# Performance work log

Hardware: AMD Instinct MI355X
Metric: run time of the kernel (lower is better)

## Reference

```python
import jax, jax.numpy as jnp
import numpy as np

H = 512   # hidden_dim
D = 512   # token feature dim (GRU input_size)
A = 256   # attn_dim
V = 10000 # vocab_size
TE = 256  # encoder timesteps
TD = 128  # decoder timesteps


def setup_inputs() -> dict:
    key = jax.random.key(0)
    ks = jax.random.split(key, 18)
    f = lambda k, shape, s: jax.random.normal(k, shape, jnp.float32) * s
    return {
        "x": f(ks[0], (1, TE, D), 1.0),
        "y": f(ks[1], (1, TD, D), 1.0),
        # encoder GRU params (PyTorch layout: gates [r|z|n] stacked)
        "Wi_e": f(ks[2], (3 * H, D), 0.04), "Wh_e": f(ks[3], (3 * H, H), 0.04),
        "bi_e": f(ks[4], (3 * H,), 0.04), "bh_e": f(ks[5], (3 * H,), 0.04),
        # decoder GRU params
        "Wi_d": f(ks[6], (3 * H, D), 0.04), "Wh_d": f(ks[7], (3 * H, H), 0.04),
        "bi_d": f(ks[8], (3 * H,), 0.04), "bh_d": f(ks[9], (3 * H,), 0.04),
        # additive attention params
        "Wh_attn": f(ks[10], (A, H), 0.06), "Ws_attn": f(ks[11], (A, H), 0.06),
        "b_attn": f(ks[12], (A,), 0.06), "v_attn": f(ks[13], (A,), 0.06),
        # output projections
        "W1": f(ks[14], (2 * V, 2 * H), 0.03), "b1": f(ks[15], (2 * V,), 0.03),
        "W2": f(ks[16], (V, 2 * V), 0.02), "b2": f(ks[17], (V,), 0.02),
    }


def _gru_gates(gi, gh, h):
    # gi/gh: [..., 3H] stacked input/hidden gate pre-activations, h: [..., H]
    ir, iz, inn = jnp.split(gi, 3, axis=-1)
    hr, hz, hn = jnp.split(gh, 3, axis=-1)
    r = jax.nn.sigmoid(ir + hr)
    z = jax.nn.sigmoid(iz + hz)
    n = jnp.tanh(inn + r * hn)
    return (1.0 - z) * n + z * h


def reference(x, y, Wi_e, Wh_e, bi_e, bh_e, Wi_d, Wh_d, bi_d, bh_d,
              Wh_attn, Ws_attn, b_attn, v_attn, W1, b1, W2, b2):
    X = x[0]  # [TE, D]
    Y = y[0]  # [TD, D]

    # Encoder: original calls self.encoder per single token with NO carried
    # hidden state, so each h_i is one GRU step from zero hidden. Vectorized:
    gi = X @ Wi_e.T + bi_e                      # [TE, 3H]
    gh = jnp.broadcast_to(bh_e, gi.shape)       # zero hidden -> only bias
    enc_H = _gru_gates(gi, gh, jnp.zeros((X.shape[0], H), X.dtype))  # [TE, H]
    h0 = enc_H[-1]                              # encoder_hidden_last

    # Decoder GRU over y with initial hidden h0
    def step(h, x_t):
        gi_t = x_t @ Wi_d.T + bi_d
        gh_t = h @ Wh_d.T + bh_d
        h_new = _gru_gates(gi_t, gh_t, h)
        return h_new, h_new

    _, dec_S = jax.lax.scan(step, h0, Y)        # [TD, H]

    # Bahdanau additive attention, fully batched over (TD, TE)
    encP = enc_H @ Wh_attn.T                    # [TE, A]
    decP = dec_S @ Ws_attn.T                    # [TD, A]
    e = jnp.tanh(encP[None, :, :] + decP[:, None, :] + b_attn)  # [TD, TE, A]
    scores = jnp.einsum('tea,a->te', e, v_attn)  # [TD, TE]
    attn = jax.nn.softmax(scores, axis=1)        # softmax over encoder steps
    context = attn @ enc_H                       # [TD, H]

    concat = jnp.concatenate([context, dec_S], axis=-1)  # [TD, 2H]
    out = concat @ W1.T + b1                     # [TD, 2V]
    out = out @ W2.T + b2                        # [TD, V]
    return out
```

## Files before the change

### kernel.cpp

```cpp
#include <hip/hip_runtime.h>
#include <stdint.h>

#define HID 512
#define THREE_H 1536
#define ADIM 256
#define NVOC 10000
#define TEnc 256
#define TDec 128

typedef float f32x4 __attribute__((ext_vector_type(4)));
typedef __bf16 bf16x8 __attribute__((ext_vector_type(8)));

__device__ __forceinline__ unsigned short f2bf(float f) {
  union { float f; unsigned u; } v; v.f = f;
  unsigned r = v.u + 0x7FFFu + ((v.u >> 16) & 1u);
  return (unsigned short)(r >> 16);
}
__device__ __forceinline__ float sigmoidf_(float x) { return 1.f / (1.f + __expf(-x)); }
__device__ __forceinline__ float tanh_fast(float x) {
  float ax = fabsf(x);
  float e = __expf(ax + ax);
  float t = 1.f - 2.f / (e + 1.f);
  return copysignf(t, x);
}

#define GLDS16(gp, lp)                                                                 \
  __builtin_amdgcn_global_load_lds((const __attribute__((address_space(1))) void*)(gp),\
                                   (__attribute__((address_space(3))) void*)(lp), 16, 0, 0)

__global__ void cvt_f32_bf16(const float* __restrict__ in, unsigned short* __restrict__ out, int n) {
  int i = (blockIdx.x * blockDim.x + threadIdx.x) * 4;
  if (i < n) {
    float4 v = *(const float4*)(in + i);
    ushort4 o;
    o.x = f2bf(v.x); o.y = f2bf(v.y); o.z = f2bf(v.z); o.w = f2bf(v.w);
    *(ushort4*)(out + i) = o;
  }
}

template <int BN, int BK>
__global__ __launch_bounds__(256, 1) void gemm_bt(
    const unsigned short* __restrict__ Abf, const float* __restrict__ B,
    const float* __restrict__ bias, float* __restrict__ C, unsigned short* __restrict__ Cbf,
    int M, int N, int K) {
  constexpr int NF = BN / 16;
  constexpr int B4 = BN * BK / 1024;
  constexpr int AG = BK / 16;
  constexpr int KK = BK / 32;
  extern __shared__ char smem[];
  unsigned short* Al0 = (unsigned short*)smem;
  unsigned short* Al1 = Al0 + 128 * BK;
  unsigned short* Bl0 = Al1 + 128 * BK;
  unsigned short* Bl1 = Bl0 + BN * BK;

  const int tid = threadIdx.x;
  const int lane = tid & 63;
  const int wid = tid >> 6;
  const int m0 = blockIdx.x * 128;
  const int n0 = blockIdx.y * BN;
  const int NT = K / BK;

  float4 breg[B4];
  f32x4 acc[2][NF];
#pragma unroll
  for (int i = 0; i < 2; ++i)
#pragma unroll
    for (int j = 0; j < NF; ++j) acc[i][j] = (f32x4){0.f, 0.f, 0.f, 0.f};

  auto stageA = [&](int t, unsigned short* dst) {
    const unsigned short* Ab = Abf + (size_t)m0 * K + (size_t)t * BK;
#pragma unroll
    for (int g = 0; g < AG; ++g) {
      int elem = g * 2048 + tid * 8;
      int arow = elem / BK;
      int acol = elem - arow * BK;
      GLDS16(Ab + (size_t)arow * K + acol, (char*)dst + g * 4096 + wid * 1024);
    }
  };
  auto loadB = [&](int t) {
    const float* Bb = B + (size_t)t * BK;
#pragma unroll
    for (int p = 0; p < B4; ++p) {
      int e = (p * 256 + tid) * 4;
      int brow = e / BK;
      int bcol = e - brow * BK;
      int grow = n0 + brow;
      if (grow > N - 1) grow = N - 1;
      breg[p] = *(const float4*)(Bb + (size_t)grow * K + bcol);
    }
  };
  auto writeB = [&](unsigned short* dst) {
#pragma unroll
    for (int p = 0; p < B4; ++p) {
      ushort4 o;
      o.x = f2bf(breg[p].x); o.y = f2bf(breg[p].y);
      o.z = f2bf(breg[p].z); o.w = f2bf(breg[p].w);
      *(ushort4*)((char*)dst + (p * 256 + tid) * 8) = o;
    }
  };

  stageA(0, Al0);
  loadB(0);
  for (int t = 0; t < NT; ++t) {
    unsigned short* Ac = (t & 1) ? Al1 : Al0;
    unsigned short* Bc = (t & 1) ? Bl1 : Bl0;
    asm volatile("s_waitcnt vmcnt(0)" ::: "memory");
    writeB(Bc);
    __syncthreads();
    if (t + 1 < NT) {
      stageA(t + 1, (t & 1) ? Al0 : Al1);
      loadB(t + 1);
    }
    const int r0 = lane & 15;
    const int kb = (lane >> 4) * 8;
#pragma unroll
    for (int kk = 0; kk < KK; ++kk) {
      int ko = kk * 32 + kb;
      bf16x8 a0 = *(const bf16x8*)(Ac + (wid * 32 + r0) * BK + ko);
      bf16x8 a1 = *(const bf16x8*)(Ac + (wid * 32 + 16 + r0) * BK + ko);
#pragma unroll
      for (int nf = 0; nf < NF; ++nf) {
        bf16x8 bb = *(const bf16x8*)(Bc + (nf * 16 + r0) * BK + ko);
        acc[0][nf] = __builtin_amdgcn_mfma_f32_16x16x32_bf16(a0, bb, acc[0][nf], 0, 0, 0);
        acc[1][nf] = __builtin_amdgcn_mfma_f32_16x16x32_bf16(a1, bb, acc[1][nf], 0, 0, 0);
      }
    }
  }
  const int cc = lane & 15;
  const int rq = (lane >> 4) * 4;
#pragma unroll
  for (int mi = 0; mi < 2; ++mi) {
    int row = m0 + wid * 32 + mi * 16 + rq;
#pragma unroll
    for (int nf = 0; nf < NF; ++nf) {
      int col = n0 + nf * 16 + cc;
      if (col < N) {
        float bv = bias ? bias[col] : 0.f;
#pragma unroll
        for (int j = 0; j < 4; ++j) {
          float v = acc[mi][nf][j] + bv;
          if (C) C[(size_t)(row + j) * N + col] = v;
          if (Cbf) Cbf[(size_t)(row + j) * N + col] = f2bf(v);
        }
      }
    }
  }
}

__global__ __launch_bounds__(256) void enc_gate(const float* __restrict__ giX,
                                                const float* __restrict__ bie,
                                                const float* __restrict__ bhe,
                                                float* __restrict__ encH,
                                                unsigned short* __restrict__ encHbf) {
  int idx = blockIdx.x * 256 + threadIdx.x;
  int i = idx >> 9, j = idx & 511;
  const float* gi = giX + (size_t)i * THREE_H;
  float r = sigmoidf_(gi[j] + bie[j] + bhe[j]);
  float z = sigmoidf_(gi[HID + j] + bie[HID + j] + bhe[HID + j]);
  float n = tanh_fast(gi[2 * HID + j] + bie[2 * HID + j] + r * bhe[2 * HID + j]);
  float h = (1.f - z) * n;
  encH[idx] = h;
  encHbf[idx] = f2bf(h);
}

__global__ __launch_bounds__(256, 1) void gru_scan_xcd(
    const float* __restrict__ Whd, const float* __restrict__ bhd,
    const float* __restrict__ giY, const float* __restrict__ h0,
    unsigned long long* __restrict__ hx, unsigned int* __restrict__ cnt,
    unsigned int* __restrict__ winner,
    unsigned short* __restrict__ decSbf, unsigned short* __restrict__ concatbf) {
  extern __shared__ char smem[];
  float* WT = (float*)smem;
  float* hl = WT + 48 * 512;
  float* dots = hl + 512;
  const int tid = threadIdx.x;
  const int lane = tid & 63, wid = tid >> 6;
  volatile int* slot_sh = (volatile int*)(dots + 52);

  if (tid == 0) {
    unsigned xcd;
    asm volatile("s_getreg_b32 %0, hwreg(20, 0, 32)" : "=s"(xcd));
    xcd &= 7u;
    unsigned slot = atomicAdd(&cnt[xcd], 1u);
    if (slot == 31u) atomicCAS(winner, 0u, xcd + 1u);
    unsigned win = 0;
    if (slot < 32u) {
      int spin = 0;
      while ((win = __hip_atomic_load(winner, __ATOMIC_RELAXED,
                                      __HIP_MEMORY_SCOPE_AGENT)) == 0u &&
             ++spin < (1 << 20))
        __builtin_amdgcn_s_sleep(2);
    }
    *slot_sh = (slot < 32u && win == xcd + 1u) ? (int)slot : -1;
  }
  __syncthreads();
  const int g = *slot_sh;
  if (g < 0) return;

  for (int idx = tid * 4; idx < 48 * 512; idx += 1024) {
    int rr = idx >> 9;
    int ccl = idx & 511;
    int grow = (rr >> 4) * HID + g * 16 + (rr & 15);
    float4 w4 = *(const float4*)(Whd + (size_t)grow * HID + ccl);
    *(float4*)(WT + ((ccl >> 2) * 48 + rr) * 4) = w4;
  }
  if (tid < 128) *(float4*)(hl + tid * 4) = *(const float4*)(h0 + tid * 4);
  __syncthreads();

  volatile unsigned long long* hxv = (volatile unsigned long long*)hx;

  for (int t = 0; t < TDec; ++t) {
    if (wid < 3) {
      int row = wid * 16 + (lane & 15);
      int q = lane >> 4;
      const float4* wp = (const float4*)WT;
      const float4* hp = (const float4*)hl;
      float p = 0.f;
#pragma unroll 8
      for (int k4 = q * 32; k4 < q * 32 + 32; ++k4) {
        float4 wv = wp[k4 * 48 + row];
        float4 hv = hp[k4];
        p += wv.x * hv.x + wv.y * hv.y + wv.z * hv.z + wv.w * hv.w;
      }
      p += __shfl_xor(p, 16);
      p += __shfl_xor(p, 32);
      if (lane < 16) dots[row] = p;
    }
    __syncthreads();
    if (tid < 16) {
      int j = g * 16 + tid;
      const float* gi = giY + (size_t)t * THREE_H;
      float r = sigmoidf_(gi[j] + dots[tid] + bhd[j]);
      float z = sigmoidf_(gi[HID + j] + dots[16 + tid] + bhd[HID + j]);
      float n = tanh_fast(gi[2 * HID + j] + r * (dots[32 + tid] + bhd[2 * HID + j]));
      float hn = (1.f - z) * n + z * hl[j];
      hxv[j] = ((unsigned long long)(unsigned)(t + 1) << 32) |
               (unsigned long long)__float_as_uint(hn);
      unsigned short hb = f2bf(hn);
      decSbf[(size_t)t * HID + j] = hb;
      concatbf[(size_t)t * 2 * HID + HID + j] = hb;
    }
    if (t == TDec - 1) break;
    __syncthreads();
    unsigned long long w0, w1;
    int spin = 0;
    do { w0 = hxv[tid]; } while ((unsigned)(w0 >> 32) != (unsigned)(t + 1) && ++spin < (1 << 16));
    spin = 0;
    do { w1 = hxv[tid + 256]; } while ((unsigned)(w1 >> 32) != (unsigned)(t + 1) && ++spin < (1 << 16));
    hl[tid] = __uint_as_float((unsigned)w0);
    hl[tid + 256] = __uint_as_float((unsigned)w1);
    __syncthreads();
  }
}

__global__ __launch_bounds__(256) void attn_ctx(const float* __restrict__ encP,
                                                const float* __restrict__ decP,
                                                const float* __restrict__ vattn,
                                                const float* __restrict__ encH,
                                                unsigned short* __restrict__ concatbf) {
  __shared__ float dp[ADIM], vv[ADIM], pl[TEnc];
  __shared__ float red[8];
  const int t = blockIdx.x, tid = threadIdx.x;
  if (tid < 64) {
    *(float4*)(dp + tid * 4) = *(const float4*)(decP + (size_t)t * ADIM + tid * 4);
    *(float4*)(vv + tid * 4) = *(const float4*)(vattn + tid * 4);
  }
  __syncthreads();
  float s = 0.f;
  const float* ep = encP + (size_t)tid * ADIM;
#pragma unroll 4
  for (int a = 0; a < ADIM; a += 4) {
    float4 e4 = *(const float4*)(ep + a);
    s += vv[a] * tanh_fast(e4.x + dp[a]);
    s += vv[a + 1] * tanh_fast(e4.y + dp[a + 1]);
    s += vv[a + 2] * tanh_fast(e4.z + dp[a + 2]);
    s += vv[a + 3] * tanh_fast(e4.w + dp[a + 3]);
  }
  float m = s;
#pragma unroll
  for (int off = 32; off; off >>= 1) m = fmaxf(m, __shfl_xor(m, off));
  if ((tid & 63) == 0) red[tid >> 6] = m;
  __syncthreads();
  m = fmaxf(fmaxf(red[0], red[1]), fmaxf(red[2], red[3]));
  float p = __expf(s - m);
  pl[tid] = p;
  float sum = p;
#pragma unroll
  for (int off = 32; off; off >>= 1) sum += __shfl_xor(sum, off);
  if ((tid & 63) == 0) red[4 + (tid >> 6)] = sum;
  __syncthreads();
  float inv = 1.f / (red[4] + red[5] + red[6] + red[7]);
  float a0 = 0.f, a1 = 0.f;
  for (int e = 0; e < TEnc; ++e) {
    float pe = pl[e];
    a0 += pe * encH[(size_t)e * HID + tid];
    a1 += pe * encH[(size_t)e * HID + tid + 256];
  }
  concatbf[(size_t)t * 2 * HID + tid] = f2bf(a0 * inv);
  concatbf[(size_t)t * 2 * HID + tid + 256] = f2bf(a1 * inv);
}

extern "C" void kernel_launch(void* const* d_in, const int* in_sizes, int n_in,
                              void* d_out, int out_size, void* d_ws, size_t ws_size,
                              hipStream_t stream) {
  const float* x = (const float*)d_in[0];
  const float* y = (const float*)d_in[1];
  const float* Wi_e = (const float*)d_in[2];
  const float* bi_e = (const float*)d_in[4];
  const float* bh_e = (const float*)d_in[5];
  const float* Wi_d = (const float*)d_in[6];
  const float* Wh_d = (const float*)d_in[7];
  const float* bi_d = (const float*)d_in[8];
  const float* bh_d = (const float*)d_in[9];
  const float* Wh_attn = (const float*)d_in[10];
  const float* Ws_attn = (const float*)d_in[11];
  const float* b_attn = (const float*)d_in[12];
  const float* v_attn = (const float*)d_in[13];
  const float* W1 = (const float*)d_in[14];
  const float* b1 = (const float*)d_in[15];
  const float* W2 = (const float*)d_in[16];
  const float* b2 = (const float*)d_in[17];
  float* out = (float*)d_out;

  char* ws = (char*)d_ws;
  size_t off = 0;
  auto alloc = [&](size_t bytes) {
    char* p = ws + off;
    off += (bytes + 255) & ~(size_t)255;
    return p;
  };
  char* ctrl = alloc(8192);
  unsigned long long* hx = (unsigned long long*)ctrl;
  unsigned int* cnt = (unsigned int*)(ctrl + 4096);
  unsigned int* winner = (unsigned int*)(ctrl + 4096 + 128);
  unsigned short* Xbf = (unsigned short*)alloc((size_t)TEnc * HID * 2);
  unsigned short* Ybf = (unsigned short*)alloc((size_t)TDec * HID * 2);
  float* giX = (float*)alloc((size_t)TEnc * THREE_H * 4);
  float* giY = (float*)alloc((size_t)TDec * THREE_H * 4);
  float* encH = (float*)alloc((size_t)TEnc * HID * 4);
  unsigned short* encHbf = (unsigned short*)alloc((size_t)TEnc * HID * 2);
  float* encP = (float*)alloc((size_t)TEnc * ADIM * 4);
  float* decP = (float*)alloc((size_t)TDec * ADIM * 4);
  unsigned short* decSbf = (unsigned short*)alloc((size_t)TDec * HID * 2);
  unsigned short* concatbf = (unsigned short*)alloc((size_t)TDec * 2 * HID * 2);
  unsigned short* out1bf = (unsigned short*)alloc((size_t)TDec * 20000 * 2);

  hipMemsetAsync(ctrl, 0, 8192, stream);

  auto* g32 = gemm_bt<32, 128>;
  auto* g80 = gemm_bt<80, 128>;
  auto* g64 = gemm_bt<64, 160>;
  const int smem32 = (128 + 32) * 128 * 2 * 2;
  const int smem80 = (128 + 80) * 128 * 2 * 2;
  const int smem64 = (128 + 64) * 160 * 2 * 2;
  const int smemScan = (48 * 512 + 512 + 64) * 4;
  hipFuncSetAttribute((const void*)g32, hipFuncAttributeMaxDynamicSharedMemorySize, smem32);
  hipFuncSetAttribute((const void*)g80, hipFuncAttributeMaxDynamicSharedMemorySize, smem80);
  hipFuncSetAttribute((const void*)g64, hipFuncAttributeMaxDynamicSharedMemorySize, smem64);
  hipFuncSetAttribute((const void*)gru_scan_xcd, hipFuncAttributeMaxDynamicSharedMemorySize, smemScan);

  cvt_f32_bf16<<<TEnc * HID / 1024, 256, 0, stream>>>(x, Xbf, TEnc * HID);
  cvt_f32_bf16<<<TDec * HID / 1024, 256, 0, stream>>>(y, Ybf, TDec * HID);

  g32<<<dim3(2, 48), 256, smem32, stream>>>(Xbf, Wi_e, nullptr, giX, nullptr, 256, 1536, 512);
  enc_gate<<<TEnc * HID / 256, 256, 0, stream>>>(giX, bi_e, bh_e, encH, encHbf);
  g32<<<dim3(2, 8), 256, smem32, stream>>>(encHbf, Wh_attn, nullptr, encP, nullptr, 256, 256, 512);
  g32<<<dim3(1, 48), 256, smem32, stream>>>(Ybf, Wi_d, bi_d, giY, nullptr, 128, 1536, 512);
  gru_scan_xcd<<<256, 256, smemScan, stream>>>(Wh_d, bh_d, giY, encH + 255 * HID,
                                               hx, cnt, winner, decSbf, concatbf);
  g32<<<dim3(1, 8), 256, smem32, stream>>>(decSbf, Ws_attn, b_attn, decP, nullptr, 128, 256, 512);
  attn_ctx<<<TDec, 256, 0, stream>>>(encP, decP, v_attn, encH, concatbf);
  g80<<<dim3(1, 250), 256, smem80, stream>>>(concatbf, W1, b1, nullptr, out1bf, 128, 20000, 1024);
  g64<<<dim3(1, 157), 256, smem64, stream>>>(out1bf, W2, b2, out, nullptr, 128, 10000, 20000);
}
```

Baseline: 664.7 us.

## Fuse encoder gates into GEMM epilogue, register-resident GRU weights, merge conversions

The encoder input GEMM now computes r/z/n columns for the same hidden units in one tile and applies the GRU gate math in its epilogue, which removes the giX intermediate and the separate enc_gate launch. The two f32→bf16 conversion launches are merged into one. The decoder scan keeps each block's Wh slice in registers instead of LDS, pads h in LDS, and hands the gate math and polling of the cross-block hidden-state exchange to a dedicated fourth wave, trimming per-step barriers. The cost is more register pressure from 32 float4 weights per lane, and the scan still requests a large dynamic LDS allocation that now goes mostly unused.

After: 753.9 us. 13.4% more time.

```diff
diff --git a/kernel.cpp b/kernel.cpp
--- a/kernel.cpp
+++ b/kernel.cpp
@@ -28,14 +28,18 @@
   __builtin_amdgcn_global_load_lds((const __attribute__((address_space(1))) void*)(gp),\
                                    (__attribute__((address_space(3))) void*)(lp), 16, 0, 0)
 
-__global__ void cvt_f32_bf16(const float* __restrict__ in, unsigned short* __restrict__ out, int n) {
+__global__ void cvt_xy(const float* __restrict__ x, const float* __restrict__ y,
+                       unsigned short* __restrict__ xb, unsigned short* __restrict__ yb) {
   int i = (blockIdx.x * blockDim.x + threadIdx.x) * 4;
-  if (i < n) {
-    float4 v = *(const float4*)(in + i);
-    ushort4 o;
-    o.x = f2bf(v.x); o.y = f2bf(v.y); o.z = f2bf(v.z); o.w = f2bf(v.w);
-    *(ushort4*)(out + i) = o;
-  }
+  const float* src;
+  unsigned short* dst;
+  int j;
+  if (i < TEnc * HID) { src = x; dst = xb; j = i; }
+  else { src = y; dst = yb; j = i - TEnc * HID; }
+  float4 v = *(const float4*)(src + j);
+  ushort4 o;
+  o.x = f2bf(v.x); o.y = f2bf(v.y); o.z = f2bf(v.z); o.w = f2bf(v.w);
+  *(ushort4*)(dst + j) = o;
 }
 
 template <int BN, int BK>
@@ -147,20 +151,112 @@
   }
 }
 
-__global__ __launch_bounds__(256) void enc_gate(const float* __restrict__ giX,
-                                                const float* __restrict__ bie,
-                                                const float* __restrict__ bhe,
-                                                float* __restrict__ encH,
-                                                unsigned short* __restrict__ encHbf) {
-  int idx = blockIdx.x * 256 + threadIdx.x;
-  int i = idx >> 9, j = idx & 511;
-  const float* gi = giX + (size_t)i * THREE_H;
-  float r = sigmoidf_(gi[j] + bie[j] + bhe[j]);
-  float z = sigmoidf_(gi[HID + j] + bie[HID + j] + bhe[HID + j]);
-  float n = tanh_fast(gi[2 * HID + j] + bie[2 * HID + j] + r * bhe[2 * HID + j]);
-  float h = (1.f - z) * n;
-  encH[idx] = h;
-  encHbf[idx] = f2bf(h);
+__global__ __launch_bounds__(256, 1) void gemm_enc(
+    const unsigned short* __restrict__ Abf, const float* __restrict__ Wi,
+    const float* __restrict__ bi, const float* __restrict__ bh,
+    float* __restrict__ encH, unsigned short* __restrict__ encHbf) {
+  constexpr int BN = 96, BK = 128, NF = 6, B4 = 12, AG = 8, KK = 4, K = 512;
+  extern __shared__ char smem[];
+  unsigned short* Al0 = (unsigned short*)smem;
+  unsigned short* Al1 = Al0 + 128 * BK;
+  unsigned short* Bl0 = Al1 + 128 * BK;
+  unsigned short* Bl1 = Bl0 + BN * BK;
+
+  const int tid = threadIdx.x;
+  const int lane = tid & 63;
+  const int wid = tid >> 6;
+  const int m0 = blockIdx.x * 128;
+  const int n0g = blockIdx.y * 32;
+  const int NT = K / BK;
+
+  float4 breg[B4];
+  f32x4 acc[2][NF];
+#pragma unroll
+  for (int i = 0; i < 2; ++i)
+#pragma unroll
+    for (int j = 0; j < NF; ++j) acc[i][j] = (f32x4){0.f, 0.f, 0.f, 0.f};
+
+  auto stageA = [&](int t, unsigned short* dst) {
+    const unsigned short* Ab = Abf + (size_t)m0 * K + (size_t)t * BK;
+#pragma unroll
+    for (int g = 0; g < AG; ++g) {
+      int elem = g * 2048 + tid * 8;
+      int arow = elem >> 7;
+      int acol = elem & 127;
+      GLDS16(Ab + (size_t)arow * K + acol, (char*)dst + g * 4096 + wid * 1024);
+    }
+  };
+  auto loadB = [&](int t) {
+    const float* Bb = Wi + (size_t)t * BK;
+#pragma unroll
+    for (int p = 0; p < B4; ++p) {
+      int e = (p * 256 + tid) * 4;
+      int brow = e >> 7;
+      int bcol = e & 127;
+      int grow = (brow >> 5) * HID + n0g + (brow & 31);
+      breg[p] = *(const float4*)(Bb + (size_t)grow * K + bcol);
+    }
+  };
+  auto writeB = [&](unsigned short* dst) {
+#pragma unroll
+    for (int p = 0; p < B4; ++p) {
+      ushort4 o;
+      o.x = f2bf(breg[p].x); o.y = f2bf(breg[p].y);
+      o.z = f2bf(breg[p].z); o.w = f2bf(breg[p].w);
+      *(ushort4*)((char*)dst + (p * 256 + tid) * 8) = o;
+    }
+  };
+
+  stageA(0, Al0);
+  loadB(0);
+  for (int t = 0; t < NT; ++t) {
+    unsigned short* Ac = (t & 1) ? Al1 : Al0;
+    unsigned short* Bc = (t & 1) ? Bl1 : Bl0;
+    asm volatile("s_waitcnt vmcnt(0)" ::: "memory");
+    writeB(Bc);
+    __syncthreads();
+    if (t + 1 < NT) {
+      stageA(t + 1, (t & 1) ? Al0 : Al1);
+      loadB(t + 1);
+    }
+    const int r0 = lane & 15;
+    const int kb = (lane >> 4) * 8;
+#pragma unroll
+    for (int kk = 0; kk < KK; ++kk) {
+      int ko = kk * 32 + kb;
+      bf16x8 a0 = *(const bf16x8*)(Ac + (wid * 32 + r0) * BK + ko);
+      bf16x8 a1 = *(const bf16x8*)(Ac + (wid * 32 + 16 + r0) * BK + ko);
+#pragma unroll
+      for (int nf = 0; nf < NF; ++nf) {
+        bf16x8 bb = *(const bf16x8*)(Bc + (nf * 16 + r0) * BK + ko);
+        acc[0][nf] = __builtin_amdgcn_mfma_f32_16x16x32_bf16(a0, bb, acc[0][nf], 0, 0, 0);
+        acc[1][nf] = __builtin_amdgcn_mfma_f32_16x16x32_bf16(a1, bb, acc[1][nf], 0, 0, 0);
+      }
+    }
+  }
+  const int cc = lane & 15;
+  const int rq = (lane >> 4) * 4;
+#pragma unroll
+  for (int mi = 0; mi < 2; ++mi) {
+    int row = m0 + wid * 32 + mi * 16 + rq;
+#pragma unroll
+    for (int nfj = 0; nfj < 2; ++nfj) {
+      int j = n0g + nfj * 16 + cc;
+      float br_ = bi[j] + bh[j];
+      float bz_ = bi[HID + j] + bh[HID + j];
+      float bin_ = bi[2 * HID + j];
+      float bhn_ = bh[2 * HID + j];
+#pragma unroll
+      for (int jj = 0; jj < 4; ++jj) {
+        float r = sigmoidf_(acc[mi][nfj][jj] + br_);
+        float z = sigmoidf_(acc[mi][nfj + 2][jj] + bz_);
+        float n = tanh_fast(acc[mi][nfj + 4][jj] + bin_ + r * bhn_);
+        float h = (1.f - z) * n;
+        encH[(size_t)(row + jj) * HID + j] = h;
+        encHbf[(size_t)(row + jj) * HID + j] = f2bf(h);
+      }
+    }
+  }
 }
 
 __global__ __launch_bounds__(256, 1) void gru_scan_xcd(
@@ -170,12 +266,11 @@
     unsigned int* __restrict__ winner,
     unsigned short* __restrict__ decSbf, unsigned short* __restrict__ concatbf) {
   extern __shared__ char smem[];
-  float* WT = (float*)smem;
-  float* hl = WT + 48 * 512;
-  float* dots = hl + 512;
+  float* hl = (float*)smem;
+  float* dots = hl + 544;
+  volatile int* slot_sh = (volatile int*)(dots + 48);
   const int tid = threadIdx.x;
   const int lane = tid & 63, wid = tid >> 6;
-  volatile int* slot_sh = (volatile int*)(dots + 52);
 
   if (tid == 0) {
     unsigned xcd;
@@ -197,59 +292,95 @@
   const int g = *slot_sh;
   if (g < 0) return;
 
-  for (int idx = tid * 4; idx < 48 * 512; idx += 1024) {
-    int rr = idx >> 9;
-    int ccl = idx & 511;
-    int grow = (rr >> 4) * HID + g * 16 + (rr & 15);
-    float4 w4 = *(const float4*)(Whd + (size_t)grow * HID + ccl);
-    *(float4*)(WT + ((ccl >> 2) * 48 + rr) * 4) = w4;
-  }
-  if (tid < 128) *(float4*)(hl + tid * 4) = *(const float4*)(h0 + tid * 4);
-  __syncthreads();
+  const int row16 = lane & 15;
+  const int q = lane >> 4;
+
+  float4 wreg[32];
+  if (wid < 3) {
+    const float* wr = Whd + ((size_t)wid * HID + (size_t)g * 16 + row16) * HID + q * 128;
+#pragma unroll
+    for (int i = 0; i < 32; ++i) wreg[i] = *(const float4*)(wr + i * 4);
+  }
+  float bhr = 0.f, bhz = 0.f, bhn = 0.f;
+  if (wid == 3 && lane < 16) {
+    int j = g * 16 + lane;
+    bhr = bhd[j]; bhz = bhd[HID + j]; bhn = bhd[2 * HID + j];
+  }
+  if (wid == 3) {
+#pragma unroll
+    for (int k = 0; k < 8; ++k) {
+      int w = lane + (k << 6);
+      hl[w + ((w >> 7) << 2)] = h0[w];
+    }
+  }
 
   volatile unsigned long long* hxv = (volatile unsigned long long*)hx;
+  float gir = 0.f, giz = 0.f, gin = 0.f;
 
   for (int t = 0; t < TDec; ++t) {
+    __syncthreads();
     if (wid < 3) {
-      int row = wid * 16 + (lane & 15);
-      int q = lane >> 4;
-      const float4* wp = (const float4*)WT;
       const float4* hp = (const float4*)hl;
-      float p = 0.f;
-#pragma unroll 8
-      for (int k4 = q * 32; k4 < q * 32 + 32; ++k4) {
-        float4 wv = wp[k4 * 48 + row];
-        float4 hv = hp[k4];
-        p += wv.x * hv.x + wv.y * hv.y + wv.z * hv.z + wv.w * hv.w;
-      }
+      const int hb = q * 33;
+      float p0 = 0.f, p1 = 0.f, p2 = 0.f, p3 = 0.f;
+#pragma unroll
+      for (int i = 0; i < 32; i += 4) {
+        float4 ha = hp[hb + i], hv = hp[hb + i + 1], hc = hp[hb + i + 2], hd = hp[hb + i + 3];
+        float4 wa = wreg[i], wb = wreg[i + 1], wc = wreg[i + 2], wd = wreg[i + 3];
+        p0 += wa.x * ha.x + wa.y * ha.y + wa.z * ha.z + wa.w * ha.w;
+        p1 += wb.x * hv.x + wb.y * hv.y + wb.z * hv.z + wb.w * hv.w;
+        p2 += wc.x * hc.x + wc.y * hc.y + wc.z * hc.z + wc.w * hc.w;
+        p3 += wd.x * hd.x + wd.y * hd.y + wd.z * hd.z + wd.w * hd.w;
+      }
+      float p = (p0 + p1) + (p2 + p3);
       p += __shfl_xor(p, 16);
       p += __shfl_xor(p, 32);
-      if (lane < 16) dots[row] = p;
+      if (lane < 16) dots[wid * 16 + lane] = p;
+    } else if (lane < 16) {
+      int j = g * 16 + lane;
+      const float* gi = giY + (size_t)t * THREE_H;
+      gir = gi[j]; giz = gi[HID + j]; gin = gi[2 * HID + j];
     }
     __syncthreads();
-    if (tid < 16) {
-      int j = g * 16 + tid;
-      const float* gi = giY + (size_t)t * THREE_H;
-      float r = sigmoidf_(gi[j] + dots[tid] + bhd[j]);
-      float z = sigmoidf_(gi[HID + j] + dots[16 + tid] + bhd[HID + j]);
-      float n = tanh_fast(gi[2 * HID + j] + r * (dots[32 + tid] + bhd[2 * HID + j]));
-      float hn = (1.f - z) * n + z * hl[j];
-      hxv[j] = ((unsigned long long)(unsigned)(t + 1) << 32) |
-               (unsigned long long)__float_as_uint(hn);
-      unsigned short hb = f2bf(hn);
-      decSbf[(size_t)t * HID + j] = hb;
-      concatbf[(size_t)t * 2 * HID + HID + j] = hb;
-    }
-    if (t == TDec - 1) break;
-    __syncthreads();
-    unsigned long long w0, w1;
-    int spin = 0;
-    do { w0 = hxv[tid]; } while ((unsigned)(w0 >> 32) != (unsigned)(t + 1) && ++spin < (1 << 16));
-    spin = 0;
-    do { w1 = hxv[tid + 256]; } while ((unsigned)(w1 >> 32) != (unsigned)(t + 1) && ++spin < (1 << 16));
-    hl[tid] = __uint_as_float((unsigned)w0);
-    hl[tid + 256] = __uint_as_float((unsigned)w1);
-    __syncthreads();
+    if (wid == 3) {
+      if (lane < 16) {
+        int j = g * 16 + lane;
+        float hprev = hl[j + ((j >> 7) << 2)];
+        float r = sigmoidf_(gir + dots[lane] + bhr);
+        float z = sigmoidf_(giz + dots[16 + lane] + bhz);
+        float n = tanh_fast(gin + r * (dots[32 + lane] + bhn));
+        float hn = (1.f - z) * n + z * hprev;
+        hxv[j] = ((unsigned long long)(unsigned)(t + 1) << 32) |
+                 (unsigned long long)__float_as_uint(hn);
+        unsigned short hb16 = f2bf(hn);
+        decSbf[(size_t)t * HID + j] = hb16;
+        concatbf[(size_t)t * 2 * HID + HID + j] = hb16;
+      }
+      if (t < TDec - 1) {
+        unsigned need = 0xFFu;
+        unsigned long long got[8];
+        got[0]=0;got[1]=0;got[2]=0;got[3]=0;got[4]=0;got[5]=0;got[6]=0;got[7]=0;
+        int guard = 0;
+        while (need && ++guard < (1 << 20)) {
+#pragma unroll
+          for (int k = 0; k < 8; ++k) {
+            if (need & (1u << k)) {
+              unsigned long long w = hxv[lane + (k << 6)];
+              if ((unsigned)(w >> 32) == (unsigned)(t + 1)) {
+                got[k] = w;
+                need &= ~(1u << k);
+              }
+            }
+          }
+          if (need) __builtin_amdgcn_s_sleep(1);
+        }
+#pragma unroll
+        for (int k = 0; k < 8; ++k) {
+          int w = lane + (k << 6);
+          hl[w + ((w >> 7) << 2)] = __uint_as_float((unsigned)got[k]);
+        }
+      }
+    }
   }
 }
 
@@ -335,7 +466,6 @@
   unsigned int* winner = (unsigned int*)(ctrl + 4096 + 128);
   unsigned short* Xbf = (unsigned short*)alloc((size_t)TEnc * HID * 2);
   unsigned short* Ybf = (unsigned short*)alloc((size_t)TDec * HID * 2);
-  float* giX = (float*)alloc((size_t)TEnc * THREE_H * 4);
   float* giY = (float*)alloc((size_t)TDec * THREE_H * 4);
   float* encH = (float*)alloc((size_t)TEnc * HID * 4);
   unsigned short* encHbf = (unsigned short*)alloc((size_t)TEnc * HID * 2);
@@ -353,17 +483,16 @@
   const int smem32 = (128 + 32) * 128 * 2 * 2;
   const int smem80 = (128 + 80) * 128 * 2 * 2;
   const int smem64 = (128 + 64) * 160 * 2 * 2;
-  const int smemScan = (48 * 512 + 512 + 64) * 4;
+  const int smemEnc = (128 + 96) * 128 * 2 * 2;
+  const int smemScan = 100608;
   hipFuncSetAttribute((const void*)g32, hipFuncAttributeMaxDynamicSharedMemorySize, smem32);
   hipFuncSetAttribute((const void*)g80, hipFuncAttributeMaxDynamicSharedMemorySize, smem80);
   hipFuncSetAttribute((const void*)g64, hipFuncAttributeMaxDynamicSharedMemorySize, smem64);
+  hipFuncSetAttribute((const void*)gemm_enc, hipFuncAttributeMaxDynamicSharedMemorySize, smemEnc);
   hipFuncSetAttribute((const void*)gru_scan_xcd, hipFuncAttributeMaxDynamicSharedMemorySize, smemScan);
 
-  cvt_f32_bf16<<<TEnc * HID / 1024, 256, 0, stream>>>(x, Xbf, TEnc * HID);
-  cvt_f32_bf16<<<TDec * HID / 1024, 256, 0, stream>>>(y, Ybf, TDec * HID);
-
-  g32<<<dim3(2, 48), 256, smem32, stream>>>(Xbf, Wi_e, nullptr, giX, nullptr, 256, 1536, 512);
-  enc_gate<<<TEnc * HID / 256, 256, 0, stream>>>(giX, bi_e, bh_e, encH, encHbf);
+  cvt_xy<<<(TEnc + TDec) * HID / 1024, 256, 0, stream>>>(x, y, Xbf, Ybf);
+  gemm_enc<<<dim3(2, 16), 256, smemEnc, stream>>>(Xbf, Wi_e, bi_e, bh_e, encH, encHbf);
   g32<<<dim3(2, 8), 256, smem32, stream>>>(encHbf, Wh_attn, nullptr, encP, nullptr, 256, 256, 512);
   g32<<<dim3(1, 48), 256, smem32, stream>>>(Ybf, Wi_d, bi_d, giY, nullptr, 128, 1536, 512);
   gru_scan_xcd<<<256, 256, smemScan, stream>>>(Wh_d, bh_d, giY, encH + 255 * HID,
```
